# Performance work log

Hardware: AMD Instinct MI355X
Metric: run time of the kernel (lower is better)

## Reference

```python
import jax, jax.numpy as jnp
import numpy as np

B, N, E, H = 4, 512, 256, 8
D = E // H


def setup_inputs() -> dict:
    key = jax.random.key(0)
    ks = jax.random.split(key, 14)
    s = 1.0 / np.sqrt(E)
    inp = {
        "query": jax.random.normal(ks[0], (B, N, E), jnp.float32),
        "attn_bias": jax.random.normal(ks[1], (B * H, N, N), jnp.float32),
        "delta_pos": jax.random.normal(ks[2], (B, N, N, 3), jnp.float32),
        "drop_edge_mask": jax.random.bernoulli(ks[3], 0.1, (N, N)),
        "Wq": jax.random.normal(ks[4], (E, E), jnp.float32) * s,
        "bq": jnp.zeros((E,), jnp.float32),
        "Wk": jax.random.normal(ks[5], (E, E), jnp.float32) * s,
        "bk": jnp.zeros((E,), jnp.float32),
        "Wv": jax.random.normal(ks[6], (E, E), jnp.float32) * s,
        "bv": jnp.zeros((E,), jnp.float32),
        "Wf1": jax.random.normal(ks[7], (1, E), jnp.float32) * s,
        "bf1": jnp.zeros((1,), jnp.float32),
        "Wf2": jax.random.normal(ks[8], (1, E), jnp.float32) * s,
        "bf2": jnp.zeros((1,), jnp.float32),
        "Wf3": jax.random.normal(ks[9], (1, E), jnp.float32) * s,
        "bf3": jnp.zeros((1,), jnp.float32),
        "drop_or_add": 1,
    }
    return inp


def reference(query, attn_bias, delta_pos, drop_edge_mask, Wq, bq, Wk, bk, Wv, bv,
              Wf1, bf1, Wf2, bf2, Wf3, bf3, drop_or_add):
    b, n, e = query.shape
    h = H
    d = e // h
    scaling = (e // h) ** (-0.5)

    def proj(W, bias):  # [b,n,e] -> [b,h,n,d]
        return (query @ W.T + bias).reshape(b, n, h, d).transpose(0, 2, 1, 3)

    q = proj(Wq, bq) * scaling
    k = proj(Wk, bk)
    v = proj(Wv, bv)

    attn = jnp.einsum('bhnd,bhmd->bhnm', q, k) + attn_bias.reshape(b, h, n, n)
    # dropout prob 0.1 in training; reference runs in eval mode (no dropout)
    probs = jax.nn.softmax(attn, axis=-1)  # [b,h,n,n]

    # outer product with 3D displacement: [b,h,n,n,3] -> [b,h,3,n,n]
    rot = probs[..., None] * delta_pos[:, None]
    rot = jnp.transpose(rot, (0, 1, 4, 2, 3))
    if drop_or_add:
        # in-place masked_fill_ in the torch code affects the final matmul
        rot = jnp.where(drop_edge_mask[None, None, None], 0.0, rot)
    # note: original code overwrites x with rot_attn_probs @ v after both
    # branches, so the 'add' branch result is discarded -- replicated here.

    # [b,h,3,n,n] @ [b,h,n,d] -> [b,n,3,h,d] -> [b,n,3,h*d]
    x = jnp.einsum('bhcnm,bhmd->bnchd', rot, v).reshape(b, n, 3, e)

    f1 = x[:, :, 0, :] @ Wf1.T + bf1
    f2 = x[:, :, 1, :] @ Wf2.T + bf2
    f3 = x[:, :, 2, :] @ Wf3.T + bf3
    return jnp.concatenate([f1, f2, f3], axis=-1).astype(jnp.float32)  # [b,n,3]
```

## Files before the change

kernel.cpp:

```cpp
#include <hip/hip_runtime.h>
#include <hip/hip_bf16.h>

#define BB 4
#define NN 512
#define EE 256
#define HH 8
#define DD 32
#define SCALING 0.17677669529663687f
#define PR 8
#define RL 8

__global__ __launch_bounds__(256) void proj_kernel(
    const float* __restrict__ query,
    const float* __restrict__ Wq, const float* __restrict__ bq,
    const float* __restrict__ Wk, const float* __restrict__ bk,
    const float* __restrict__ Wv, const float* __restrict__ bv,
    const float* __restrict__ Wf1, const float* __restrict__ Wf2,
    const float* __restrict__ Wf3,
    float* __restrict__ Q, float* __restrict__ Kt, float* __restrict__ vw)
{
    __shared__ alignas(16) float s[PR][EE];
    __shared__ alignas(16) float sv[PR][EE];
    const int which = blockIdx.y;
    const int row0 = blockIdx.x * PR;
    const int tid = threadIdx.x;

    {
        const float4* src = (const float4*)(query + row0 * EE);
        ((float4*)s)[tid]       = src[tid];
        ((float4*)s)[tid + 256] = src[tid + 256];
    }
    __syncthreads();

    const float* W  = (which == 0) ? Wq : (which == 1) ? Wk : Wv;
    const float* bb = (which == 0) ? bq : (which == 1) ? bk : bv;

    float acc[PR];
    #pragma unroll
    for (int r = 0; r < PR; ++r) acc[r] = 0.f;

    const float4* W4 = (const float4*)(W + tid * EE);
    for (int j = 0; j < EE / 4; ++j) {
        const float4 w = W4[j];
        #pragma unroll
        for (int r = 0; r < PR; ++r) {
            const float4 x = *(const float4*)&s[r][4 * j];
            acc[r] += x.x * w.x + x.y * w.y + x.z * w.z + x.w * w.w;
        }
    }
    const float bbv = bb[tid];

    if (which == 0) {
        #pragma unroll
        for (int r = 0; r < PR; ++r)
            Q[(row0 + r) * EE + tid] = (acc[r] + bbv) * SCALING;
    } else if (which == 1) {
        const int h = tid >> 5, d = tid & 31;
        #pragma unroll
        for (int r = 0; r < PR; ++r) {
            const int grow = row0 + r;
            const int b = grow >> 9, n = grow & 511;
            Kt[((size_t)(b * HH + h) * DD + d) * NN + n] = acc[r] + bbv;
        }
    } else {
        #pragma unroll
        for (int r = 0; r < PR; ++r) sv[r][tid] = acc[r] + bbv;
        __syncthreads();
        if (tid < PR * 24) {
            const int r = tid / 24;
            const int rem = tid % 24;
            const int hh = rem / 3;
            const int c = rem % 3;
            const float* Wf = (c == 0) ? Wf1 : (c == 1) ? Wf2 : Wf3;
            float a = 0.f;
            #pragma unroll
            for (int dd = 0; dd < DD; ++dd)
                a += sv[r][hh * DD + dd] * Wf[hh * DD + dd];
            const int grow = row0 + r;
            const int b = grow >> 9, m = grow & 511;
            vw[((b * HH + hh) * 3 + c) * NN + m] = a;
        }
    }
}

__global__ __launch_bounds__(512) void logits_kernel(
    const float* __restrict__ Q, const float* __restrict__ Kt,
    const float* __restrict__ attn_bias,
    __hip_bfloat16* __restrict__ Pp, float* __restrict__ Spart)
{
    const int blk = blockIdx.x;
    const int b = blk >> 6;
    const int n0 = (blk & 63) * RL;
    const int h = blockIdx.y;
    const int m = threadIdx.x;
    const int wv = m >> 6, ln = m & 63;

    const float* kp = Kt + ((size_t)(b * HH + h) * DD) * NN + m;
    float kreg[DD];
    #pragma unroll
    for (int d = 0; d < DD; ++d) kreg[d] = kp[(size_t)d * NN];

    const size_t bias_base = ((size_t)(b * HH + h) * NN + n0) * NN + m;
    const float* qb = Q + (b * NN + n0) * EE + h * DD;

    #pragma unroll
    for (int r = 0; r < RL; ++r) {
        float l = attn_bias[bias_base + (size_t)r * NN];
        #pragma unroll
        for (int d = 0; d < DD; ++d)
            l += qb[r * EE + d] * kreg[d];
        const float e = __expf(l);

        Pp[((size_t)(b * HH + h) * NN + (n0 + r)) * NN + m] =
            __float2bfloat16(e);

        float x = e;
        #pragma unroll
        for (int off = 32; off; off >>= 1)
            x += __shfl_xor(x, off, 64);
        if (ln == 0)
            Spart[((size_t)(b * HH + h) * NN + (n0 + r)) * 8 + wv] = x;
    }
}

__global__ __launch_bounds__(512) void contract_kernel(
    const __hip_bfloat16* __restrict__ Pp, const float* __restrict__ Spart,
    const float* __restrict__ vw, const float* __restrict__ delta_pos,
    const int* __restrict__ drop_edge_mask, const int* __restrict__ drop_or_add,
    const float* __restrict__ bf1, const float* __restrict__ bf2,
    const float* __restrict__ bf3, float* __restrict__ out)
{
    const int blk = blockIdx.x;
    const int b = blk >> 9, n = blk & 511;
    const int m = threadIdx.x;
    const int wv_id = m >> 6, ln = m & 63;

    __shared__ float sred[64];
    __shared__ float srcp[HH];
    __shared__ float r3[3][8];
    __shared__ float sdp[3 * NN];

    {
        const float* dpb = delta_pos + (size_t)(b * NN + n) * NN * 3;
        sdp[m]        = dpb[m];
        sdp[m + 512]  = dpb[m + 512];
        sdp[m + 1024] = dpb[m + 1024];
    }
    if (m < 64)
        sred[m] = Spart[((size_t)(b * HH + (m >> 3)) * NN + n) * 8 + (m & 7)];
    __syncthreads();
    if (m < HH) {
        float s = 0.f;
        #pragma unroll
        for (int w = 0; w < 8; ++w) s += sred[m * 8 + w];
        srcp[m] = __builtin_amdgcn_rcpf(s);
    }
    __syncthreads();

    float A0 = 0.f, A1 = 0.f, A2 = 0.f;
    #pragma unroll
    for (int h = 0; h < HH; ++h) {
        const float p =
            __bfloat162float(Pp[((size_t)(b * HH + h) * NN + n) * NN + m]) *
            srcp[h];
        const float* vwp = vw + (b * HH + h) * 3 * NN + m;
        A0 += p * vwp[0];
        A1 += p * vwp[NN];
        A2 += p * vwp[2 * NN];
    }

    const float mk =
        (drop_or_add[0] != 0 && drop_edge_mask[n * NN + m] != 0) ? 0.f : 1.f;
    float v0 = A0 * sdp[3 * m + 0] * mk;
    float v1 = A1 * sdp[3 * m + 1] * mk;
    float v2 = A2 * sdp[3 * m + 2] * mk;
    #pragma unroll
    for (int off = 32; off; off >>= 1) {
        v0 += __shfl_xor(v0, off, 64);
        v1 += __shfl_xor(v1, off, 64);
        v2 += __shfl_xor(v2, off, 64);
    }
    if (ln == 0) { r3[0][wv_id] = v0; r3[1][wv_id] = v1; r3[2][wv_id] = v2; }
    __syncthreads();

    if (m < 3) {
        float s = 0.f;
        #pragma unroll
        for (int w = 0; w < 8; ++w) s += r3[m][w];
        const float bias = (m == 0) ? bf1[0] : (m == 1) ? bf2[0] : bf3[0];
        out[(b * NN + n) * 3 + m] = s + bias;
    }
}

extern "C" void kernel_launch(void* const* d_in, const int* in_sizes, int n_in,
                              void* d_out, int out_size, void* d_ws, size_t ws_size,
                              hipStream_t stream)
{
    const float* query          = (const float*)d_in[0];
    const float* attn_bias      = (const float*)d_in[1];
    const float* delta_pos      = (const float*)d_in[2];
    const int*   drop_edge_mask = (const int*)d_in[3];
    const float* Wq  = (const float*)d_in[4];
    const float* bq  = (const float*)d_in[5];
    const float* Wk  = (const float*)d_in[6];
    const float* bk  = (const float*)d_in[7];
    const float* Wv  = (const float*)d_in[8];
    const float* bv  = (const float*)d_in[9];
    const float* Wf1 = (const float*)d_in[10];
    const float* bf1 = (const float*)d_in[11];
    const float* Wf2 = (const float*)d_in[12];
    const float* bf2 = (const float*)d_in[13];
    const float* Wf3 = (const float*)d_in[14];
    const float* bf3 = (const float*)d_in[15];
    const int*   drop_or_add = (const int*)d_in[16];

    float* ws = (float*)d_ws;
    float* Q     = ws;
    float* Kt    = ws + 524288;
    float* vw    = ws + 1048576;
    float* Spart = ws + 1097728;
    __hip_bfloat16* Pp = (__hip_bfloat16*)(ws + 1228800);

    proj_kernel<<<dim3(BB * NN / PR, 3), 256, 0, stream>>>(
        query, Wq, bq, Wk, bk, Wv, bv, Wf1, Wf2, Wf3, Q, Kt, vw);
    logits_kernel<<<dim3(BB * NN / RL, HH), 512, 0, stream>>>(
        Q, Kt, attn_bias, Pp, Spart);
    contract_kernel<<<BB * NN, 512, 0, stream>>>(Pp, Spart, vw, delta_pos,
                                                 drop_edge_mask, drop_or_add,
                                                 bf1, bf2, bf3, (float*)d_out);
}
```

Before: 64.44 us.

## Recompute softmax sums in contract kernel with per-head waves and vector loads

Removes the per-row shuffle reduction and Spart partial-sum writes from the logits kernel. The contract kernel now assigns one wave per head and 8 columns per lane, computing the row sum from the bf16 probabilities directly. It uses 128-bit vector loads for probabilities, vw, delta_pos and mask, and drops the shared-memory staging and one barrier. Each wave redundantly loads the same delta_pos and mask slice, and the normalizer now comes from rounded bf16 values.

```diff
diff --git a/kernel.cpp b/kernel.cpp
--- a/kernel.cpp
+++ b/kernel.cpp
@@ -9,6 +9,13 @@
 #define SCALING 0.17677669529663687f
 #define PR 8
 #define RL 8
+
+__device__ __forceinline__ float bf16lo(unsigned u) {
+    return __uint_as_float(u << 16);
+}
+__device__ __forceinline__ float bf16hi(unsigned u) {
+    return __uint_as_float(u & 0xffff0000u);
+}
 
 __global__ __launch_bounds__(256) void proj_kernel(
     const float* __restrict__ query,
@@ -86,14 +93,13 @@
 __global__ __launch_bounds__(512) void logits_kernel(
     const float* __restrict__ Q, const float* __restrict__ Kt,
     const float* __restrict__ attn_bias,
-    __hip_bfloat16* __restrict__ Pp, float* __restrict__ Spart)
+    __hip_bfloat16* __restrict__ Pp)
 {
     const int blk = blockIdx.x;
     const int b = blk >> 6;
     const int n0 = (blk & 63) * RL;
     const int h = blockIdx.y;
     const int m = threadIdx.x;
-    const int wv = m >> 6, ln = m & 63;
 
     const float* kp = Kt + ((size_t)(b * HH + h) * DD) * NN + m;
     float kreg[DD];
@@ -110,85 +116,96 @@
         for (int d = 0; d < DD; ++d)
             l += qb[r * EE + d] * kreg[d];
         const float e = __expf(l);
-
         Pp[((size_t)(b * HH + h) * NN + (n0 + r)) * NN + m] =
             __float2bfloat16(e);
-
-        float x = e;
-        #pragma unroll
-        for (int off = 32; off; off >>= 1)
-            x += __shfl_xor(x, off, 64);
-        if (ln == 0)
-            Spart[((size_t)(b * HH + h) * NN + (n0 + r)) * 8 + wv] = x;
     }
 }
 
 __global__ __launch_bounds__(512) void contract_kernel(
-    const __hip_bfloat16* __restrict__ Pp, const float* __restrict__ Spart,
-    const float* __restrict__ vw, const float* __restrict__ delta_pos,
+    const __hip_bfloat16* __restrict__ Pp, const float* __restrict__ vw,
+    const float* __restrict__ delta_pos,
     const int* __restrict__ drop_edge_mask, const int* __restrict__ drop_or_add,
     const float* __restrict__ bf1, const float* __restrict__ bf2,
     const float* __restrict__ bf3, float* __restrict__ out)
 {
     const int blk = blockIdx.x;
     const int b = blk >> 9, n = blk & 511;
-    const int m = threadIdx.x;
-    const int wv_id = m >> 6, ln = m & 63;
-
-    __shared__ float sred[64];
-    __shared__ float srcp[HH];
-    __shared__ float r3[3][8];
-    __shared__ float sdp[3 * NN];
-
-    {
-        const float* dpb = delta_pos + (size_t)(b * NN + n) * NN * 3;
-        sdp[m]        = dpb[m];
-        sdp[m + 512]  = dpb[m + 512];
-        sdp[m + 1024] = dpb[m + 1024];
-    }
-    if (m < 64)
-        sred[m] = Spart[((size_t)(b * HH + (m >> 3)) * NN + n) * 8 + (m & 7)];
+    const int tid = threadIdx.x;
+    const int w = __builtin_amdgcn_readfirstlane(tid >> 6);
+    const int ln = tid & 63;
+    const int m8 = ln * 8;
+
+    __shared__ float r3[HH][3];
+
+    const uint4 pu =
+        *(const uint4*)(Pp + ((size_t)(b * HH + w) * NN + n) * NN + m8);
+    float p[8];
+    p[0] = bf16lo(pu.x); p[1] = bf16hi(pu.x);
+    p[2] = bf16lo(pu.y); p[3] = bf16hi(pu.y);
+    p[4] = bf16lo(pu.z); p[5] = bf16hi(pu.z);
+    p[6] = bf16lo(pu.w); p[7] = bf16hi(pu.w);
+
+    float S = ((p[0] + p[1]) + (p[2] + p[3])) + ((p[4] + p[5]) + (p[6] + p[7]));
+    #pragma unroll
+    for (int off = 32; off; off >>= 1)
+        S += __shfl_xor(S, off, 64);
+    const float srcp = __builtin_amdgcn_rcpf(S);
+
+    const float* vwb = vw + (size_t)(b * HH + w) * 3 * NN + m8;
+    const float4 va0 = *(const float4*)(vwb);
+    const float4 va1 = *(const float4*)(vwb + 4);
+    const float4 vb0 = *(const float4*)(vwb + NN);
+    const float4 vb1 = *(const float4*)(vwb + NN + 4);
+    const float4 vc0 = *(const float4*)(vwb + 2 * NN);
+    const float4 vc1 = *(const float4*)(vwb + 2 * NN + 4);
+
+    const float* dpb = delta_pos + ((size_t)(b * NN + n) * NN + m8) * 3;
+    const float4 q0 = *(const float4*)(dpb);
+    const float4 q1 = *(const float4*)(dpb + 4);
+    const float4 q2 = *(const float4*)(dpb + 8);
+    const float4 q3 = *(const float4*)(dpb + 12);
+    const float4 q4 = *(const float4*)(dpb + 16);
+    const float4 q5 = *(const float4*)(dpb + 20);
+
+    const int4 mk0 = *(const int4*)(drop_edge_mask + n * NN + m8);
+    const int4 mk1 = *(const int4*)(drop_edge_mask + n * NN + m8 + 4);
+    const int doa = drop_or_add[0];
+
+    float sc[8];
+    sc[0] = (doa && mk0.x) ? 0.f : p[0] * srcp;
+    sc[1] = (doa && mk0.y) ? 0.f : p[1] * srcp;
+    sc[2] = (doa && mk0.z) ? 0.f : p[2] * srcp;
+    sc[3] = (doa && mk0.w) ? 0.f : p[3] * srcp;
+    sc[4] = (doa && mk1.x) ? 0.f : p[4] * srcp;
+    sc[5] = (doa && mk1.y) ? 0.f : p[5] * srcp;
+    sc[6] = (doa && mk1.z) ? 0.f : p[6] * srcp;
+    sc[7] = (doa && mk1.w) ? 0.f : p[7] * srcp;
+
+    float t0, t1, t2;
+    t0  = sc[0] * q0.x * va0.x;  t1  = sc[0] * q0.y * vb0.x;  t2  = sc[0] * q0.z * vc0.x;
+    t0 += sc[1] * q0.w * va0.y;  t1 += sc[1] * q1.x * vb0.y;  t2 += sc[1] * q1.y * vc0.y;
+    t0 += sc[2] * q1.z * va0.z;  t1 += sc[2] * q1.w * vb0.z;  t2 += sc[2] * q2.x * vc0.z;
+    t0 += sc[3] * q2.y * va0.w;  t1 += sc[3] * q2.z * vb0.w;  t2 += sc[3] * q2.w * vc0.w;
+    t0 += sc[4] * q3.x * va1.x;  t1 += sc[4] * q3.y * vb1.x;  t2 += sc[4] * q3.z * vc1.x;
+    t0 += sc[5] * q3.w * va1.y;  t1 += sc[5] * q4.x * vb1.y;  t2 += sc[5] * q4.y * vc1.y;
+    t0 += sc[6] * q4.z * va1.z;  t1 += sc[6] * q4.w * vb1.z;  t2 += sc[6] * q5.x * vc1.z;
+    t0 += sc[7] * q5.y * va1.w;  t1 += sc[7] * q5.z * vb1.w;  t2 += sc[7] * q5.w * vc1.w;
+
+    #pragma unroll
+    for (int off = 32; off; off >>= 1) {
+        t0 += __shfl_xor(t0, off, 64);
+        t1 += __shfl_xor(t1, off, 64);
+        t2 += __shfl_xor(t2, off, 64);
+    }
+    if (ln == 0) { r3[w][0] = t0; r3[w][1] = t1; r3[w][2] = t2; }
     __syncthreads();
-    if (m < HH) {
+
+    if (tid < 3) {
         float s = 0.f;
         #pragma unroll
-        for (int w = 0; w < 8; ++w) s += sred[m * 8 + w];
-        srcp[m] = __builtin_amdgcn_rcpf(s);
-    }
-    __syncthreads();
-
-    float A0 = 0.f, A1 = 0.f, A2 = 0.f;
-    #pragma unroll
-    for (int h = 0; h < HH; ++h) {
-        const float p =
-            __bfloat162float(Pp[((size_t)(b * HH + h) * NN + n) * NN + m]) *
-            srcp[h];
-        const float* vwp = vw + (b * HH + h) * 3 * NN + m;
-        A0 += p * vwp[0];
-        A1 += p * vwp[NN];
-        A2 += p * vwp[2 * NN];
-    }
-
-    const float mk =
-        (drop_or_add[0] != 0 && drop_edge_mask[n * NN + m] != 0) ? 0.f : 1.f;
-    float v0 = A0 * sdp[3 * m + 0] * mk;
-    float v1 = A1 * sdp[3 * m + 1] * mk;
-    float v2 = A2 * sdp[3 * m + 2] * mk;
-    #pragma unroll
-    for (int off = 32; off; off >>= 1) {
-        v0 += __shfl_xor(v0, off, 64);
-        v1 += __shfl_xor(v1, off, 64);
-        v2 += __shfl_xor(v2, off, 64);
-    }
-    if (ln == 0) { r3[0][wv_id] = v0; r3[1][wv_id] = v1; r3[2][wv_id] = v2; }
-    __syncthreads();
-
-    if (m < 3) {
-        float s = 0.f;
-        #pragma unroll
-        for (int w = 0; w < 8; ++w) s += r3[m][w];
-        const float bias = (m == 0) ? bf1[0] : (m == 1) ? bf2[0] : bf3[0];
-        out[(b * NN + n) * 3 + m] = s + bias;
+        for (int hh = 0; hh < HH; ++hh) s += r3[hh][tid];
+        const float bias = (tid == 0) ? bf1[0] : (tid == 1) ? bf2[0] : bf3[0];
+        out[(b * NN + n) * 3 + tid] = s + bias;
     }
 }
 
@@ -215,17 +232,16 @@
     const int*   drop_or_add = (const int*)d_in[16];
 
     float* ws = (float*)d_ws;
-    float* Q     = ws;
-    float* Kt    = ws + 524288;
-    float* vw    = ws + 1048576;
-    float* Spart = ws + 1097728;
+    float* Q   = ws;
+    float* Kt  = ws + 524288;
+    float* vw  = ws + 1048576;
     __hip_bfloat16* Pp = (__hip_bfloat16*)(ws + 1228800);
 
     proj_kernel<<<dim3(BB * NN / PR, 3), 256, 0, stream>>>(
         query, Wq, bq, Wk, bk, Wv, bv, Wf1, Wf2, Wf3, Q, Kt, vw);
     logits_kernel<<<dim3(BB * NN / RL, HH), 512, 0, stream>>>(
-        Q, Kt, attn_bias, Pp, Spart);
-    contract_kernel<<<BB * NN, 512, 0, stream>>>(Pp, Spart, vw, delta_pos,
+        Q, Kt, attn_bias, Pp);
+    contract_kernel<<<BB * NN, 512, 0, stream>>>(Pp, vw, delta_pos,
                                                  drop_edge_mask, drop_or_add,
                                                  bf1, bf2, bf3, (float*)d_out);
 }
```

Result: slower. 66.16 us (+2.7%).

## Fuse logits and contraction into one kernel with per-head atomic output accumulation

Applied to the files above, without the earlier changes.

Merges the logits kernel and the contraction kernel, so each block computes the exp-logits, the softmax denominator, and the masked delta_pos and vw contraction for its rows and head. The per-head results are then added into the output with atomics. This removes the bf16 probability buffer write and reread, the partial-sum buffer and one kernel launch. In exchange, delta_pos is now read once per head (8x redundant), the output needs a memset, and RL is halved, which adds blocks and K-register reloads.

```diff
diff --git a/kernel.cpp b/kernel.cpp
--- a/kernel.cpp
+++ b/kernel.cpp
@@ -8,7 +8,7 @@
 #define DD 32
 #define SCALING 0.17677669529663687f
 #define PR 8
-#define RL 8
+#define RL 4
 
 __global__ __launch_bounds__(256) void proj_kernel(
     const float* __restrict__ query,
@@ -83,17 +83,22 @@
     }
 }
 
-__global__ __launch_bounds__(512) void logits_kernel(
+__global__ __launch_bounds__(512) void fused_attn_kernel(
     const float* __restrict__ Q, const float* __restrict__ Kt,
-    const float* __restrict__ attn_bias,
-    __hip_bfloat16* __restrict__ Pp, float* __restrict__ Spart)
+    const float* __restrict__ attn_bias, const float* __restrict__ vw,
+    const float* __restrict__ delta_pos,
+    const int* __restrict__ drop_edge_mask, const int* __restrict__ drop_or_add,
+    const float* __restrict__ bf1, const float* __restrict__ bf2,
+    const float* __restrict__ bf3, float* __restrict__ out)
 {
-    const int blk = blockIdx.x;
-    const int b = blk >> 6;
-    const int n0 = (blk & 63) * RL;
+    const int bx = blockIdx.x;
+    const int b = bx >> 7;
+    const int n0 = (bx & 127) * RL;
     const int h = blockIdx.y;
     const int m = threadIdx.x;
     const int wv = m >> 6, ln = m & 63;
+
+    __shared__ float red[RL][4][8];
 
     const float* kp = Kt + ((size_t)(b * HH + h) * DD) * NN + m;
     float kreg[DD];
@@ -103,6 +108,10 @@
     const size_t bias_base = ((size_t)(b * HH + h) * NN + n0) * NN + m;
     const float* qb = Q + (b * NN + n0) * EE + h * DD;
 
+    const float* vwb = vw + (size_t)(b * HH + h) * 3 * NN + m;
+    const float vw0 = vwb[0], vw1 = vwb[NN], vw2 = vwb[2 * NN];
+    const int doa = drop_or_add[0];
+
     #pragma unroll
     for (int r = 0; r < RL; ++r) {
         float l = attn_bias[bias_base + (size_t)r * NN];
@@ -111,84 +120,49 @@
             l += qb[r * EE + d] * kreg[d];
         const float e = __expf(l);
 
-        Pp[((size_t)(b * HH + h) * NN + (n0 + r)) * NN + m] =
-            __float2bfloat16(e);
-
-        float x = e;
-        #pragma unroll
-        for (int off = 32; off; off >>= 1)
-            x += __shfl_xor(x, off, 64);
-        if (ln == 0)
-            Spart[((size_t)(b * HH + h) * NN + (n0 + r)) * 8 + wv] = x;
-    }
-}
-
-__global__ __launch_bounds__(512) void contract_kernel(
-    const __hip_bfloat16* __restrict__ Pp, const float* __restrict__ Spart,
-    const float* __restrict__ vw, const float* __restrict__ delta_pos,
-    const int* __restrict__ drop_edge_mask, const int* __restrict__ drop_or_add,
-    const float* __restrict__ bf1, const float* __restrict__ bf2,
-    const float* __restrict__ bf3, float* __restrict__ out)
-{
-    const int blk = blockIdx.x;
-    const int b = blk >> 9, n = blk & 511;
-    const int m = threadIdx.x;
-    const int wv_id = m >> 6, ln = m & 63;
-
-    __shared__ float sred[64];
-    __shared__ float srcp[HH];
-    __shared__ float r3[3][8];
-    __shared__ float sdp[3 * NN];
-
-    {
-        const float* dpb = delta_pos + (size_t)(b * NN + n) * NN * 3;
-        sdp[m]        = dpb[m];
-        sdp[m + 512]  = dpb[m + 512];
-        sdp[m + 1024] = dpb[m + 1024];
-    }
-    if (m < 64)
-        sred[m] = Spart[((size_t)(b * HH + (m >> 3)) * NN + n) * 8 + (m & 7)];
+        const float mk =
+            (doa != 0 && drop_edge_mask[(n0 + r) * NN + m] != 0) ? 0.f : 1.f;
+        const float* dp = delta_pos + ((size_t)(b * NN + (n0 + r)) * NN + m) * 3;
+        const float t = e * mk;
+        float v0 = t * dp[0] * vw0;
+        float v1 = t * dp[1] * vw1;
+        float v2 = t * dp[2] * vw2;
+        float vs = e;
+
+        #pragma unroll
+        for (int off = 32; off; off >>= 1) {
+            v0 += __shfl_xor(v0, off, 64);
+            v1 += __shfl_xor(v1, off, 64);
+            v2 += __shfl_xor(v2, off, 64);
+            vs += __shfl_xor(vs, off, 64);
+        }
+        if (ln == 0) {
+            red[r][0][wv] = v0;
+            red[r][1][wv] = v1;
+            red[r][2][wv] = v2;
+            red[r][3][wv] = vs;
+        }
+    }
     __syncthreads();
-    if (m < HH) {
-        float s = 0.f;
-        #pragma unroll
-        for (int w = 0; w < 8; ++w) s += sred[m * 8 + w];
-        srcp[m] = __builtin_amdgcn_rcpf(s);
-    }
-    __syncthreads();
-
-    float A0 = 0.f, A1 = 0.f, A2 = 0.f;
-    #pragma unroll
-    for (int h = 0; h < HH; ++h) {
-        const float p =
-            __bfloat162float(Pp[((size_t)(b * HH + h) * NN + n) * NN + m]) *
-            srcp[h];
-        const float* vwp = vw + (b * HH + h) * 3 * NN + m;
-        A0 += p * vwp[0];
-        A1 += p * vwp[NN];
-        A2 += p * vwp[2 * NN];
-    }
-
-    const float mk =
-        (drop_or_add[0] != 0 && drop_edge_mask[n * NN + m] != 0) ? 0.f : 1.f;
-    float v0 = A0 * sdp[3 * m + 0] * mk;
-    float v1 = A1 * sdp[3 * m + 1] * mk;
-    float v2 = A2 * sdp[3 * m + 2] * mk;
-    #pragma unroll
-    for (int off = 32; off; off >>= 1) {
-        v0 += __shfl_xor(v0, off, 64);
-        v1 += __shfl_xor(v1, off, 64);
-        v2 += __shfl_xor(v2, off, 64);
-    }
-    if (ln == 0) { r3[0][wv_id] = v0; r3[1][wv_id] = v1; r3[2][wv_id] = v2; }
-    __syncthreads();
-
-    if (m < 3) {
-        float s = 0.f;
-        #pragma unroll
-        for (int w = 0; w < 8; ++w) s += r3[m][w];
-        const float bias = (m == 0) ? bf1[0] : (m == 1) ? bf2[0] : bf3[0];
-        out[(b * NN + n) * 3 + m] = s + bias;
+
+    if (m < RL) {
+        const int r = m;
+        float T0 = 0.f, T1 = 0.f, T2 = 0.f, S = 0.f;
+        #pragma unroll
+        for (int w = 0; w < 8; ++w) {
+            T0 += red[r][0][w];
+            T1 += red[r][1][w];
+            T2 += red[r][2][w];
+            S  += red[r][3][w];
+        }
+        const float rcpS = __builtin_amdgcn_rcpf(S);
+        float* o = out + (size_t)(b * NN + n0 + r) * 3;
+        const float a0 = T0 * rcpS + ((h == 0) ? bf1[0] : 0.f);
+        const float a1 = T1 * rcpS + ((h == 0) ? bf2[0] : 0.f);
+        const float a2 = T2 * rcpS + ((h == 0) ? bf3[0] : 0.f);
+        atomicAdd(o + 0, a0);
+        atomicAdd(o + 1, a1);
+        atomicAdd(o + 2, a2);
     }
 }
 
@@ -215,17 +189,15 @@
     const int*   drop_or_add = (const int*)d_in[16];
 
     float* ws = (float*)d_ws;
-    float* Q     = ws;
-    float* Kt    = ws + 524288;
-    float* vw    = ws + 1048576;
-    float* Spart = ws + 1097728;
-    __hip_bfloat16* Pp = (__hip_bfloat16*)(ws + 1228800);
+    float* Q   = ws;
+    float* Kt  = ws + 524288;
+    float* vw  = ws + 1048576;
+
+    hipMemsetAsync(d_out, 0, (size_t)out_size * sizeof(float), stream);
 
     proj_kernel<<<dim3(BB * NN / PR, 3), 256, 0, stream>>>(
         query, Wq, bq, Wk, bk, Wv, bv, Wf1, Wf2, Wf3, Q, Kt, vw);
-    logits_kernel<<<dim3(BB * NN / RL, HH), 512, 0, stream>>>(
-        Q, Kt, attn_bias, Pp, Spart);
-    contract_kernel<<<BB * NN, 512, 0, stream>>>(Pp, Spart, vw, delta_pos,
-                                                 drop_edge_mask, drop_or_add,
-                                                 bf1, bf2, bf3, (float*)d_out);
+    fused_attn_kernel<<<dim3(BB * NN / RL, HH), 512, 0, stream>>>(
+        Q, Kt, attn_bias, vw, delta_pos, drop_edge_mask, drop_or_add,
+        bf1, bf2, bf3, (float*)d_out);
 }
```

Result: slower. 78.01 us (+21.1%).
